# Performance work log

Hardware: AMD Instinct MI355X
Metric: run time of the kernel (lower is better)

The kernel has to match this reference:

```python
import jax, jax.numpy as jnp
import numpy as np

B, N, C, O, K, D = 32, 2048, 64, 64, 3, 16

def setup_inputs() -> dict:
    key = jax.random.key(0)
    ks = jax.random.split(key, 6)
    x = jax.random.normal(ks[0], (B, N, C), dtype=jnp.float32)
    node_embeddings = jax.random.normal(ks[1], (N, D), dtype=jnp.float32)
    adj_m = jax.random.uniform(ks[2], (N, N), dtype=jnp.float32)
    weights_pool = jax.random.normal(ks[3], (D, K, C, O), dtype=jnp.float32) * 0.1
    bias_pool = jax.random.normal(ks[4], (D, O), dtype=jnp.float32) * 0.1
    sa_weight = jax.random.normal(ks[5], (N, 2 * N), dtype=jnp.float32) * (1.0 / np.sqrt(2 * N))
    return {"x": x, "node_embeddings": node_embeddings, "adj_m": adj_m,
            "weights_pool": weights_pool, "bias_pool": bias_pool, "sa_weight": sa_weight}

def reference(x, node_embeddings, adj_m, weights_pool, bias_pool, sa_weight):
    n = node_embeddings.shape[0]
    # learned adaptive adjacency [N,N]
    supports = jax.nn.softmax(jax.nn.relu(node_embeddings @ node_embeddings.T), axis=1)
    # SpatialAttention: 1x1 conv over 2N channels == matmul with [N,2N] weight
    z = jnp.concatenate([supports, adj_m], axis=1) @ sa_weight.T  # [N,N]
    s2 = jax.nn.sigmoid(z)
    supports = s2 * adj_m + (1.0 - s2) * supports
    # Chebyshev polynomial basis
    support_set = [jnp.eye(n, dtype=supports.dtype), supports]
    for _ in range(2, K):
        support_set.append(2.0 * supports @ support_set[-1] - support_set[-2])
    supports_k = jnp.stack(support_set, axis=0)  # [K,N,N]
    # per-node generated weights/bias from embeddings
    weights = jnp.einsum('nd,dkio->nkio', node_embeddings, weights_pool)  # [N,K,C,O]
    bias = node_embeddings @ bias_pool  # [N,O]
    # graph conv: aggregate then per-node matmul
    x_g = jnp.einsum('knm,bmc->bnkc', supports_k, x)  # [B,N,K,C]
    x_gconv = jnp.einsum('bnki,nkio->bno', x_g, weights) + bias  # [B,N,O]
    return x_gconv
```

## Files before the change

kernel.cpp:

```cpp
#include <hip/hip_runtime.h>


typedef unsigned short u16;
typedef float f32x4 __attribute__((ext_vector_type(4)));
typedef __bf16 bf16x8 __attribute__((ext_vector_type(8)));
typedef unsigned short u16x8 __attribute__((ext_vector_type(8)));

#define PSTRIDE ((size_t)2048 * 2048)

__device__ __forceinline__ u16 f2bf(float f) {
    unsigned u = __float_as_uint(f);
    u += 0x7FFFu + ((u >> 16) & 1u);
    return (u16)(u >> 16);
}
__device__ __forceinline__ float bf2f(u16 h) {
    return __uint_as_float((unsigned)h << 16);
}
__device__ __forceinline__ void gl_lds16(const void* g, void* l) {
    __builtin_amdgcn_global_load_lds(
        (const __attribute__((address_space(1))) unsigned*)g,
        (__attribute__((address_space(3))) unsigned*)l, 16, 0, 0);
}

__global__ __launch_bounds__(256)
void preA(const float* __restrict__ E, const float* __restrict__ adj,
          const float* __restrict__ saw, const float* __restrict__ x,
          const float* __restrict__ Wp, const float* __restrict__ bp,
          u16* __restrict__ Acat, u16* __restrict__ sawb, u16* __restrict__ xtT,
          u16* __restrict__ Wpb, float* __restrict__ Wpbf,
          float* __restrict__ bias, u16* __restrict__ xn, int mode) {
    __shared__ __align__(16) char smem[32768];
    const int bid = blockIdx.x, tid = threadIdx.x;

    if (bid < 256) {
        float* Et4 = (float*)smem;
        const int r0 = bid * 8;
        float z[8][8] = {};
#pragma unroll
        for (int ph = 0; ph < 4; ++ph) {
            if (ph) __syncthreads();
#pragma unroll
            for (int k = 0; k < 8; ++k) {
                const int n = tid + 256 * k;
                float4 e = ((const float4*)(E + (size_t)n * 16))[ph];
                Et4[0 * 2048 + n] = e.x; Et4[1 * 2048 + n] = e.y;
                Et4[2 * 2048 + n] = e.z; Et4[3 * 2048 + n] = e.w;
            }
            __syncthreads();
#pragma unroll
            for (int d = 0; d < 4; ++d) {
                const float* row = Et4 + d * 2048;
                float ev[8];
#pragma unroll
                for (int k = 0; k < 8; ++k) ev[k] = row[tid + 256 * k];
#pragma unroll
                for (int r = 0; r < 8; ++r) {
                    float e = row[r0 + r];
#pragma unroll
                    for (int k = 0; k < 8; ++k) z[r][k] = fmaf(e, ev[k], z[r][k]);
                }
            }
        }
        __syncthreads();
        float (*redm)[8] = (float(*)[8])smem;
        float (*reds)[8] = (float(*)[8])(smem + 256);

        float mr[8];
#pragma unroll
        for (int r = 0; r < 8; ++r) {
            float m = 0.f;
#pragma unroll
            for (int k = 0; k < 8; ++k) { z[r][k] = fmaxf(z[r][k], 0.f); m = fmaxf(m, z[r][k]); }
            mr[r] = m;
        }
#pragma unroll
        for (int off = 32; off; off >>= 1)
#pragma unroll
            for (int r = 0; r < 8; ++r) mr[r] = fmaxf(mr[r], __shfl_xor(mr[r], off, 64));
        if ((tid & 63) == 0) {
#pragma unroll
            for (int r = 0; r < 8; ++r) redm[tid >> 6][r] = mr[r];
        }
        __syncthreads();
#pragma unroll
        for (int r = 0; r < 8; ++r)
            mr[r] = fmaxf(fmaxf(redm[0][r], redm[1][r]), fmaxf(redm[2][r], redm[3][r]));
        float sr[8];
#pragma unroll
        for (int r = 0; r < 8; ++r) {
            float s = 0.f;
#pragma unroll
            for (int k = 0; k < 8; ++k) { z[r][k] = __expf(z[r][k] - mr[r]); s += z[r][k]; }
            sr[r] = s;
        }
#pragma unroll
        for (int off = 32; off; off >>= 1)
#pragma unroll
            for (int r = 0; r < 8; ++r) sr[r] += __shfl_xor(sr[r], off, 64);
        if ((tid & 63) == 0) {
#pragma unroll
            for (int r = 0; r < 8; ++r) reds[tid >> 6][r] = sr[r];
        }
        __syncthreads();
#pragma unroll
        for (int r = 0; r < 8; ++r) {
            float inv = 1.f / (reds[0][r] + reds[1][r] + reds[2][r] + reds[3][r]);
            u16* orow = Acat + (size_t)(r0 + r) * 4096;
#pragma unroll
            for (int k = 0; k < 8; ++k) orow[tid + 256 * k] = f2bf(z[r][k] * inv);
        }
    } else if (bid < 1792) {
        const size_t NADJ = 1048576, STRIDE = (size_t)1536 * 256;
        const size_t e0 = (size_t)(bid - 256) * 256 + tid;
        float4 v[8];
#pragma unroll
        for (int it = 0; it < 8; ++it) {
            size_t idx = e0 + (size_t)it * STRIDE;
            const float* src = (idx < NADJ) ? (adj + idx * 4) : (saw + (idx - NADJ) * 4);
            v[it] = *(const float4*)src;
        }
#pragma unroll
        for (int it = 0; it < 8; ++it) {
            size_t idx = e0 + (size_t)it * STRIDE;
            ushort4 o = make_ushort4(f2bf(v[it].x), f2bf(v[it].y), f2bf(v[it].z), f2bf(v[it].w));
            if (idx < NADJ) {
                size_t j = idx * 4;
                int n = (int)(j >> 11), c = (int)(j & 2047);
                *(ushort4*)(Acat + (size_t)n * 4096 + 2048 + c) = o;
            } else {
                *(ushort4*)(sawb + (idx - NADJ) * 4) = o;
            }
        }
    } else if (bid < 2816) {
        u16 (*t)[65] = (u16(*)[65])smem;
        int local = bid - 1792;
        int m0 = (local & 31) * 64, b = local >> 5;
        int c = tid & 63, g = tid >> 6;
#pragma unroll
        for (int r = 0; r < 16; ++r) {
            int mm = g * 16 + r;
            t[mm][c] = f2bf(x[((size_t)b * 2048 + m0 + mm) * 64 + c]);
        }
        __syncthreads();
#pragma unroll
        for (int r = 0; r < 16; ++r) {
            int cc = g * 16 + r;
            xtT[((size_t)b * 64 + cc) * 2048 + m0 + c] = t[c][cc];
        }
        if (mode) {
#pragma unroll
            for (int r = 0; r < 16; ++r) {
                int mm = g * 16 + r;
                xn[((size_t)(m0 + mm)) * 2048 + b * 64 + c] = t[mm][c];
            }
        }
    } else if (bid < 2832) {
        float (*tw)[97] = (float(*)[97])smem;
        const int d = bid - 2816;
        const float* base = Wp + (size_t)d * 12288;
        const int o = tid & 63, seg = tid >> 6;
#pragma unroll
        for (int half = 0; half < 2; ++half) {
            if (half) __syncthreads();
#pragma unroll
            for (int j = 0; j < 24; ++j) {
                int ki = half * 96 + seg * 24 + j;
                int k = ki >> 6, i = ki & 63;
                float v;
                if (k == 0)      v = base[i * 64 + o] - base[8192 + i * 64 + o];
                else if (k == 1) v = base[4096 + i * 64 + o];
                else             v = 2.f * base[8192 + i * 64 + o];
                tw[o][ki - half * 96] = v;
            }
            __syncthreads();
#pragma unroll
            for (int it = 0; it < 6; ++it) {
                int idx = tid + it * 256;
                int oo = idx / 24, q = idx - oo * 24;
                float v0 = tw[oo][q * 4], v1 = tw[oo][q * 4 + 1];
                float v2 = tw[oo][q * 4 + 2], v3 = tw[oo][q * 4 + 3];
                size_t dst = (size_t)(d * 64 + oo) * 192 + half * 96 + q * 4;
                *(float4*)(Wpbf + dst) = make_float4(v0, v1, v2, v3);
                *(ushort4*)(Wpb + dst) = make_ushort4(f2bf(v0), f2bf(v1), f2bf(v2), f2bf(v3));
            }
        }
    } else {
        const int nb = bid - 2832;
#pragma unroll
        for (int it = 0; it < 8; ++it) {
            int idx = tid + it * 256;
            int n = nb * 32 + (idx >> 6), o = idx & 63;
            float s = 0.f;
#pragma unroll
            for (int d = 0; d < 16; ++d) s = fmaf(E[n * 16 + d], bp[d * 64 + o], s);
            bias[(size_t)n * 64 + o] = s;
        }
    }
}

__global__ __launch_bounds__(256)
void rzmid(const u16* __restrict__ p, const u16* __restrict__ Acat,
           u16* __restrict__ S, const float* __restrict__ E,
           const float* __restrict__ Wpbf, u16* __restrict__ Wnb) {
    __shared__ float Es[32 * 16];
    const int bid = blockIdx.x, tid = threadIdx.x;
    if (bid < 1024) {
        const size_t base = ((size_t)bid * 256 + tid) * 4;
        const size_t STRIDE = (size_t)1024 * 256 * 4;
#pragma unroll
        for (int it = 0; it < 4; ++it) {
            size_t j = base + (size_t)it * STRIDE;
            ushort4 p0 = *(const ushort4*)(p + j);
            ushort4 p1 = *(const ushort4*)(p + PSTRIDE + j);
            ushort4 p2 = *(const ushort4*)(p + 2 * PSTRIDE + j);
            ushort4 p3 = *(const ushort4*)(p + 3 * PSTRIDE + j);
            int row = (int)(j >> 11), col = (int)(j & 2047);
            ushort4 sp = *(const ushort4*)(Acat + (size_t)row * 4096 + col);
            ushort4 ad = *(const ushort4*)(Acat + (size_t)row * 4096 + 2048 + col);
            float z0 = bf2f(p0.x) + bf2f(p1.x) + bf2f(p2.x) + bf2f(p3.x);
            float z1 = bf2f(p0.y) + bf2f(p1.y) + bf2f(p2.y) + bf2f(p3.y);
            float z2 = bf2f(p0.z) + bf2f(p1.z) + bf2f(p2.z) + bf2f(p3.z);
            float z3 = bf2f(p0.w) + bf2f(p1.w) + bf2f(p2.w) + bf2f(p3.w);
            float s0 = 1.f / (1.f + __expf(-z0)), s1 = 1.f / (1.f + __expf(-z1));
            float s2 = 1.f / (1.f + __expf(-z2)), s3 = 1.f / (1.f + __expf(-z3));
            ushort4 o = make_ushort4(
                f2bf(s0 * bf2f(ad.x) + (1.f - s0) * bf2f(sp.x)),
                f2bf(s1 * bf2f(ad.y) + (1.f - s1) * bf2f(sp.y)),
                f2bf(s2 * bf2f(ad.z) + (1.f - s2) * bf2f(sp.z)),
                f2bf(s3 * bf2f(ad.w) + (1.f - s3) * bf2f(sp.w)));
            *(ushort4*)(S + j) = o;
        }
    } else {
        const int w = bid - 1024;
        const int c0 = (w % 12) * 1024, n0 = (w / 12) * 32;
        for (int j = tid; j < 512; j += 256) Es[j] = E[(size_t)n0 * 16 + j];
        float4 wf[16];
#pragma unroll
        for (int d = 0; d < 16; ++d)
            wf[d] = *(const float4*)(Wpbf + (size_t)d * 12288 + c0 + tid * 4);
        __syncthreads();
        for (int nl = 0; nl < 32; ++nl) {
            float4 s = make_float4(0.f, 0.f, 0.f, 0.f);
#pragma unroll
            for (int d = 0; d < 16; ++d) {
                float e = Es[nl * 16 + d];
                s.x = fmaf(e, wf[d].x, s.x);
                s.y = fmaf(e, wf[d].y, s.y);
                s.z = fmaf(e, wf[d].z, s.z);
                s.w = fmaf(e, wf[d].w, s.w);
            }
            *(ushort4*)(Wnb + (size_t)(n0 + nl) * 12288 + c0 + tid * 4) =
                make_ushort4(f2bf(s.x), f2bf(s.y), f2bf(s.z), f2bf(s.w));
        }
    }
}

__global__ __launch_bounds__(512, 2)
void gemm_bt256(const u16* __restrict__ A, const u16* __restrict__ Bt,
                u16* __restrict__ Cp, int M, int N, int K, int Kh) {
    __shared__ alignas(16) u16 As[2][256 * 64];
    __shared__ alignas(16) u16 Bs[2][256 * 64];
    const int tid = threadIdx.x, lane = tid & 63, wave = tid >> 6;

    const int nbx = gridDim.x, nby = gridDim.y, nbz = gridDim.z;
    const int nwg = nbx * nby * nbz;
    int lin = (blockIdx.z * nby + blockIdx.y) * nbx + blockIdx.x;
    if ((nwg & 7) == 0) lin = (lin & 7) * (nwg >> 3) + (lin >> 3);
    const int bz = lin / (nbx * nby);
    const int r2 = lin - bz * nbx * nby;
    const int by = r2 / nbx, bx = r2 - by * nbx;

    const int m0 = by * 256, n0 = bx * 256;
    const int kbeg = bz * Kh;
    const int NT = Kh >> 6;
    const int wm = (wave >> 2) * 128, wn = (wave & 3) * 64;
    const int ml = lane & 15, c0l = lane >> 4;

    int sI[4], rowI[4], gcI[4];
#pragma unroll
    for (int r = 0; r < 4; ++r) {
        int s = r * 512 + tid;
        sI[r] = s; rowI[r] = s >> 3; gcI[r] = (s & 7) ^ ((s >> 3) & 7);
    }

    f32x4 acc[8][4] = {};
    bf16x8 af[4][2], bv[2][2];

#define LOADA(r_, kt_, buf_) \
    gl_lds16(A + (size_t)(m0 + rowI[r_]) * K + (kt_) + gcI[r_] * 8, \
             &As[buf_][sI[r_] * 8])
#define LOADB(r_, kt_, buf_) \
    gl_lds16(Bt + (size_t)(n0 + rowI[r_]) * K + (kt_) + gcI[r_] * 8, \
             &Bs[buf_][sI[r_] * 8])

#define DSRA(qa_) \
    _Pragma("unroll") \
    for (int i = 0; i < 4; ++i) { \
        const int mr = wm + (qa_) * 64 + i * 16 + ml; \
        _Pragma("unroll") \
        for (int ks = 0; ks < 2; ++ks) \
            af[i][ks] = *(const bf16x8*)(Asc + mr * 64 + (((c0l + ks * 4) ^ (mr & 7)) * 8)); \
    }
#define DSRB(qb_) \
    _Pragma("unroll") \
    for (int j = 0; j < 2; ++j) { \
        const int nr = wn + (qb_) * 32 + j * 16 + ml; \
        _Pragma("unroll") \
        for (int ks = 0; ks < 2; ++ks) \
            bv[j][ks] = *(const bf16x8*)(Bsc + nr * 64 + (((c0l + ks * 4) ^ (nr & 7)) * 8)); \
    }
#define MMQ(io_, jo_) \
    __builtin_amdgcn_s_barrier(); \
    asm volatile("s_waitcnt lgkmcnt(0)" ::: "memory"); \
    __builtin_amdgcn_s_setprio(1); \
    _Pragma("unroll") \
    for (int ks = 0; ks < 2; ++ks) \
        _Pragma("unroll") \
        for (int i = 0; i < 4; ++i) \
            _Pragma("unroll") \
            for (int j = 0; j < 2; ++j) \
                acc[(io_) + i][(jo_) + j] = __builtin_amdgcn_mfma_f32_16x16x32_bf16( \
                    af[i][ks], bv[j][ks], acc[(io_) + i][(jo_) + j], 0, 0, 0); \
    __builtin_amdgcn_s_setprio(0);

#pragma unroll
    for (int r = 0; r < 4; ++r) LOADA(r, kbeg, 0);
#pragma unroll
    for (int r = 0; r < 4; ++r) LOADB(r, kbeg, 0);
    asm volatile("s_waitcnt vmcnt(0)" ::: "memory");
    __builtin_amdgcn_s_barrier();

    for (int t = 0; t < NT - 1; ++t) {
        const int cur = t & 1, nxt = cur ^ 1;
        const u16* Asc = As[cur];
        const u16* Bsc = Bs[cur];
        const int k1 = kbeg + (t + 1) * 64;

        DSRA(0); DSRB(0);
        LOADB(0, k1, nxt); LOADB(1, k1, nxt);
        MMQ(0, 0);
        __builtin_amdgcn_s_barrier();

        DSRB(1);
        LOADB(2, k1, nxt); LOADB(3, k1, nxt);
        MMQ(0, 2);
        asm volatile("s_waitcnt vmcnt(4)" ::: "memory");
        __builtin_amdgcn_s_barrier();

        DSRA(1);
        LOADA(0, k1, nxt); LOADA(2, k1, nxt);
        MMQ(4, 2);
        __builtin_amdgcn_s_barrier();

        DSRB(0);
        LOADA(1, k1, nxt); LOADA(3, k1, nxt);
        MMQ(4, 0);
        asm volatile("s_waitcnt vmcnt(2)" ::: "memory");
        __builtin_amdgcn_s_barrier();
    }

    {
        const int cur = (NT - 1) & 1;
        const u16* Asc = As[cur];
        const u16* Bsc = Bs[cur];

        DSRA(0); DSRB(0);
        MMQ(0, 0);
        __builtin_amdgcn_s_barrier();

        DSRB(1);
        MMQ(0, 2);
        asm volatile("s_waitcnt vmcnt(0)" ::: "memory");
        __builtin_amdgcn_s_barrier();

        DSRA(1);
        MMQ(4, 2);
        __builtin_amdgcn_s_barrier();

        DSRB(0);
        MMQ(4, 0);
    }

#undef LOADA
#undef LOADB
#undef DSRA
#undef DSRB
#undef MMQ

    const int col_l = lane & 15, rl = (lane >> 4) * 4;
    u16* Cz = Cp + (size_t)bz * M * N;
#pragma unroll
    for (int i = 0; i < 8; ++i)
#pragma unroll
        for (int j = 0; j < 4; ++j)
#pragma unroll
            for (int r = 0; r < 4; ++r) {
                int row = m0 + wm + i * 16 + rl + r;
                int col = n0 + wn + j * 16 + col_l;
                Cz[(size_t)row * N + col] = f2bf(acc[i][j][r]);
            }
}

__global__ __launch_bounds__(256)
void reduceT(const u16* __restrict__ p, u16* __restrict__ xg1o,
             u16* __restrict__ xg1T, int mode) {
    __shared__ u16 t[64][68];
    int bx = blockIdx.x * 64, by = blockIdx.y * 64;
    int cg = threadIdx.x & 15, rg = threadIdx.x >> 4;
    int b = bx >> 6;
#pragma unroll
    for (int rr = 0; rr < 4; ++rr) {
        int row = rg * 4 + rr;
        size_t idx = (size_t)(by + row) * 2048 + bx + cg * 4;
        ushort4 q0 = *(const ushort4*)(p + idx);
        ushort4 q1 = *(const ushort4*)(p + PSTRIDE + idx);
        ushort4 q2 = *(const ushort4*)(p + 2 * PSTRIDE + idx);
        ushort4 q3 = *(const ushort4*)(p + 3 * PSTRIDE + idx);
        ushort4 v = make_ushort4(
            f2bf(bf2f(q0.x) + bf2f(q1.x) + bf2f(q2.x) + bf2f(q3.x)),
            f2bf(bf2f(q0.y) + bf2f(q1.y) + bf2f(q2.y) + bf2f(q3.y)),
            f2bf(bf2f(q0.z) + bf2f(q1.z) + bf2f(q2.z) + bf2f(q3.z)),
            f2bf(bf2f(q0.w) + bf2f(q1.w) + bf2f(q2.w) + bf2f(q3.w)));
        if (mode) *(ushort4*)(xg1o + idx) = v;
        else      *(ushort4*)(xg1o + ((size_t)b * 2048 + by + row) * 64 + cg * 4) = v;
        *(ushort4*)(&t[row][cg * 4]) = v;
    }
    __syncthreads();
    int c = threadIdx.x & 63, g = threadIdx.x >> 6;
#pragma unroll
    for (int r = 0; r < 16; ++r) {
        int row = g * 16 + r;
        xg1T[(size_t)(bx + row) * 2048 + by + c] = t[c][row];
    }
}

__global__ __launch_bounds__(256, 4)
void gconv_wn(const u16* __restrict__ xn, const u16* __restrict__ xg1n,
              const u16* __restrict__ p, const u16* __restrict__ Wnb,
              const float* __restrict__ bias, float* __restrict__ out) {
    __shared__ alignas(16) u16 As[32 * 192];
    __shared__ alignas(16) u16 Bs[64 * 192];
    const int n = blockIdx.x, tid = threadIdx.x;
    const int lane = tid & 63, wave = tid >> 6;
    const int wn2 = wave * 16;
    const int ml = lane & 15, c0l = lane >> 4;
    const int col = lane & 15, rl = (lane >> 4) * 4;

#pragma unroll
    for (int it = 0; it < 6; ++it) {
        int s = tid + it * 256;
        int row = s / 24, sc = s - row * 24;
        int gc = (sc & 24) | ((sc ^ row) & 7);
        gl_lds16(Wnb + (size_t)n * 12288 + (size_t)row * 192 + gc * 8, Bs + (size_t)s * 8);
    }
#pragma unroll
    for (int it = 0; it < 3; ++it) {
        int s = tid + it * 256;
        int row = s / 24, sc = s - row * 24;
        int gc = (sc & 24) | ((sc ^ row) & 7);
        u16x8 v;
        if (gc < 8) {
            v = *(const u16x8*)(xn + (size_t)n * 2048 + row * 64 + (gc & 7) * 8);
        } else if (gc < 16) {
            v = *(const u16x8*)(xg1n + (size_t)n * 2048 + row * 64 + (gc & 7) * 8);
        } else {
            const u16* pp = p + (size_t)n * 2048 + row * 64 + (gc & 7) * 8;
            u16x8 q0 = *(const u16x8*)pp;
            u16x8 q1 = *(const u16x8*)(pp + PSTRIDE);
            u16x8 q2 = *(const u16x8*)(pp + 2 * PSTRIDE);
            u16x8 q3 = *(const u16x8*)(pp + 3 * PSTRIDE);
#pragma unroll
            for (int tt = 0; tt < 8; ++tt)
                v[tt] = f2bf(bf2f(q0[tt]) + bf2f(q1[tt]) + bf2f(q2[tt]) + bf2f(q3[tt]));
        }
        *(u16x8*)(As + (size_t)s * 8) = v;
    }
    float bv0 = bias[(size_t)n * 64 + wn2 + col];
    f32x4 acc[2];
#pragma unroll
    for (int mt = 0; mt < 2; ++mt)
#pragma unroll
        for (int r = 0; r < 4; ++r) acc[mt][r] = bv0;
    __syncthreads();

#pragma unroll
    for (int ks = 0; ks < 6; ++ks) {
        int c = c0l + ks * 4;
        int o = wn2 + ml;
        bf16x8 bfrag = *(const bf16x8*)(Bs + (o * 24 + ((c & 24) | ((c ^ (o & 7)) & 7))) * 8);
#pragma unroll
        for (int mt = 0; mt < 2; ++mt) {
            int m = mt * 16 + ml;
            bf16x8 afrag = *(const bf16x8*)(As + (m * 24 + ((c & 24) | ((c ^ (m & 7)) & 7))) * 8);
            acc[mt] = __builtin_amdgcn_mfma_f32_16x16x32_bf16(afrag, bfrag, acc[mt], 0, 0, 0);
        }
    }
#pragma unroll
    for (int mt = 0; mt < 2; ++mt)
#pragma unroll
        for (int r = 0; r < 4; ++r) {
            int b = mt * 16 + rl + r;
            out[((size_t)b * 2048 + n) * 64 + wn2 + col] = acc[mt][r];
        }
}

__global__ __launch_bounds__(256, 2)
void gconv_mfma(const float* __restrict__ x, const u16* __restrict__ xg1,
                const u16* __restrict__ p, const u16* __restrict__ Wpb,
                const float* __restrict__ bias, const float* __restrict__ E,
                float* __restrict__ out) {
    __shared__ alignas(16) float El[16 * 128];
    const int tid = threadIdx.x, lane = tid & 63, wave = tid >> 6;
    const int m0 = blockIdx.x * 128, nb = m0 & 2047, bB = m0 >> 11;
    const int wm = (wave >> 1) * 64, wn = (wave & 1) * 32;
    const int ml = lane & 15, c0l = lane >> 4;
    const int col_l = lane & 15, rl = (lane >> 4) * 4;

#pragma unroll
    for (int it = 0; it < 8; ++it) {
        int idx = tid + it * 256;
        El[idx] = E[(size_t)(nb + (idx & 127)) * 16 + (idx >> 7)];
    }
    __syncthreads();

    bf16x8 af[4][6];
#pragma unroll
    for (int i = 0; i < 4; ++i) {
        const int row = m0 + wm + i * 16 + ml;
        const int n = row & 2047;
#pragma unroll
        for (int ks = 0; ks < 2; ++ks) {
            const float* xp = x + (size_t)row * 64 + (c0l + ks * 4) * 8;
            float4 a = *(const float4*)xp, b4 = *(const float4*)(xp + 4);
            u16x8 v;
            v[0] = f2bf(a.x);  v[1] = f2bf(a.y);  v[2] = f2bf(a.z);  v[3] = f2bf(a.w);
            v[4] = f2bf(b4.x); v[5] = f2bf(b4.y); v[6] = f2bf(b4.z); v[7] = f2bf(b4.w);
            af[i][ks] = __builtin_bit_cast(bf16x8, v);
        }
#pragma unroll
        for (int ks = 2; ks < 4; ++ks)
            af[i][ks] = *(const bf16x8*)(xg1 + (size_t)row * 64 + (c0l + ks * 4 - 8) * 8);
#pragma unroll
        for (int ks = 4; ks < 6; ++ks) {
            const u16* pp = p + (size_t)n * 2048 + bB * 64 + (c0l + ks * 4 - 16) * 8;
            u16x8 q0 = *(const u16x8*)pp;
            u16x8 q1 = *(const u16x8*)(pp + PSTRIDE);
            u16x8 q2 = *(const u16x8*)(pp + 2 * PSTRIDE);
            u16x8 q3 = *(const u16x8*)(pp + 3 * PSTRIDE);
            u16x8 v;
#pragma unroll
            for (int tt = 0; tt < 8; ++tt)
                v[tt] = f2bf(bf2f(q0[tt]) + bf2f(q1[tt]) + bf2f(q2[tt]) + bf2f(q3[tt]));
            af[i][ks] = __builtin_bit_cast(bf16x8, v);
        }
    }

    f32x4 oacc[4][2];
#pragma unroll
    for (int i = 0; i < 4; ++i)
#pragma unroll
        for (int j = 0; j < 2; ++j)
#pragma unroll
            for (int r = 0; r < 4; ++r)
                oacc[i][j][r] = bias[(size_t)(nb + wm + i * 16 + rl + r) * 64 + wn + j * 16 + col_l];

#pragma unroll 2
    for (int d = 0; d < 16; ++d) {
        bf16x8 bv[2][6];
#pragma unroll
        for (int j = 0; j < 2; ++j) {
            const u16* wp = Wpb + (size_t)(d * 64 + wn + j * 16 + ml) * 192 + c0l * 8;
#pragma unroll
            for (int ks = 0; ks < 6; ++ks)
                bv[j][ks] = *(const bf16x8*)(wp + ks * 32);
        }
        f32x4 tmp[4][2] = {};
#pragma unroll
        for (int ks = 0; ks < 6; ++ks)
#pragma unroll
            for (int i = 0; i < 4; ++i)
#pragma unroll
                for (int j = 0; j < 2; ++j)
                    tmp[i][j] = __builtin_amdgcn_mfma_f32_16x16x32_bf16(af[i][ks], bv[j][ks], tmp[i][j], 0, 0, 0);
#pragma unroll
        for (int i = 0; i < 4; ++i) {
            f32x4 ev = *(const f32x4*)(El + d * 128 + wm + i * 16 + rl);
#pragma unroll
            for (int r = 0; r < 4; ++r)
#pragma unroll
                for (int j = 0; j < 2; ++j)
                    oacc[i][j][r] = fmaf(ev[r], tmp[i][j][r], oacc[i][j][r]);
        }
    }
#pragma unroll
    for (int i = 0; i < 4; ++i)
#pragma unroll
        for (int j = 0; j < 2; ++j)
#pragma unroll
            for (int r = 0; r < 4; ++r)
                out[(size_t)(m0 + wm + i * 16 + rl + r) * 64 + wn + j * 16 + col_l] = oacc[i][j][r];
}

extern "C" void kernel_launch(void* const* d_in, const int* in_sizes, int n_in,
                              void* d_out, int out_size, void* d_ws, size_t ws_size,
                              hipStream_t stream) {
    const float* x   = (const float*)d_in[0];
    const float* E   = (const float*)d_in[1];
    const float* adj = (const float*)d_in[2];
    const float* Wp  = (const float*)d_in[3];
    const float* bp  = (const float*)d_in[4];
    const float* saw = (const float*)d_in[5];
    float* out = (float*)d_out;

    char* ws = (char*)d_ws;
    const size_t MB = 1u << 20;
    const int wn_mode = (ws_size >= 140 * MB) ? 1 : 0;

    u16*   Acat  = (u16*)(ws);
    u16*   sawb  = (u16*)(ws + 16 * MB);
    u16*   XtT   = (u16*)(ws + 32 * MB);
    u16*   Wpb   = (u16*)(ws + 40 * MB);
    float* bias  = (float*)(ws + 41 * MB);
    float* Wpbf  = (float*)(ws + 42 * MB);
    u16*   part  = (u16*)(ws + 48 * MB);
    u16*   S_bf  = (u16*)(ws + 16 * MB);
    u16*   xg1T  = (u16*)(ws + 24 * MB);
    u16*   xg1o  = (u16*)(ws);
    u16*   xn    = (u16*)(ws + 80 * MB);
    u16*   Wnb   = (u16*)(ws + 88 * MB);

    preA<<<2896, 256, 0, stream>>>(E, adj, saw, x, Wp, bp, Acat, sawb, XtT,
                                   Wpb, Wpbf, bias, xn, wn_mode);

    gemm_bt256<<<dim3(8, 8, 4), 512, 0, stream>>>(Acat, sawb, part, 2048, 2048, 4096, 1024);
    rzmid<<<wn_mode ? 1792 : 1024, 256, 0, stream>>>(part, Acat, S_bf, E, Wpbf, Wnb);
    gemm_bt256<<<dim3(8, 8, 4), 512, 0, stream>>>(S_bf, XtT, part, 2048, 2048, 2048, 512);
    reduceT<<<dim3(32, 32), 256, 0, stream>>>(part, xg1o, xg1T, wn_mode);
    gemm_bt256<<<dim3(8, 8, 4), 512, 0, stream>>>(S_bf, xg1T, part, 2048, 2048, 2048, 512);

    if (wn_mode)
        gconv_wn<<<2048, 256, 0, stream>>>(xn, xg1o, part, Wnb, bias, out);
    else
        gconv_mfma<<<512, 256, 0, stream>>>(x, xg1o, part, Wpb, bias, E, out);
}
```

Baseline: 274.7 us.

## Split preprocessing kernel into memory-bound and compute-bound kernels, move Wnb generation earlier

Moves the embedding softmax work and the per-node weight generation (Wnb) out of the mixed preprocessing and reduction kernels into a new kernel, zsmW, launched before the first GEMM. The remaining conversion work goes into preB, which uses less LDS and a 4-blocks-per-CU launch bound so more blocks can be resident, and it processes more elements per block in the adj/saw conversion. The sigmoid-blend reduction becomes a lean standalone kernel. This adds one kernel launch in exchange for better occupancy and less branch divergence across heterogeneous blocks.

```diff
diff --git a/kernel.cpp b/kernel.cpp
--- a/kernel.cpp
+++ b/kernel.cpp
@@ -22,105 +22,70 @@
         (__attribute__((address_space(3))) unsigned*)l, 16, 0, 0);
 }
 
-__global__ __launch_bounds__(256)
-void preA(const float* __restrict__ E, const float* __restrict__ adj,
+__global__ __launch_bounds__(256, 4)
+void preB(const float* __restrict__ E, const float* __restrict__ adj,
           const float* __restrict__ saw, const float* __restrict__ x,
           const float* __restrict__ Wp, const float* __restrict__ bp,
           u16* __restrict__ Acat, u16* __restrict__ sawb, u16* __restrict__ xtT,
           u16* __restrict__ Wpb, float* __restrict__ Wpbf,
           float* __restrict__ bias, u16* __restrict__ xn, int mode) {
-    __shared__ __align__(16) char smem[32768];
+    __shared__ __align__(16) char smem[12800];
     const int bid = blockIdx.x, tid = threadIdx.x;
 
-    if (bid < 256) {
-        float* Et4 = (float*)smem;
-        const int r0 = bid * 8;
-        float z[8][8] = {};
-#pragma unroll
-        for (int ph = 0; ph < 4; ++ph) {
-            if (ph) __syncthreads();
-#pragma unroll
-            for (int k = 0; k < 8; ++k) {
-                const int n = tid + 256 * k;
-                float4 e = ((const float4*)(E + (size_t)n * 16))[ph];
-                Et4[0 * 2048 + n] = e.x; Et4[1 * 2048 + n] = e.y;
-                Et4[2 * 2048 + n] = e.z; Et4[3 * 2048 + n] = e.w;
+    if (bid < 16) {
+        float (*tw)[49] = (float(*)[49])smem;
+        const int d = bid;
+        const float* base = Wp + (size_t)d * 12288;
+        const int o = tid & 63, seg = tid >> 6;
+#pragma unroll
+        for (int p = 0; p < 4; ++p) {
+            if (p) __syncthreads();
+#pragma unroll
+            for (int j = 0; j < 12; ++j) {
+                int kil = seg * 12 + j;
+                int ki = p * 48 + kil;
+                int k = ki >> 6, i = ki & 63;
+                float v;
+                if (k == 0)      v = base[i * 64 + o] - base[8192 + i * 64 + o];
+                else if (k == 1) v = base[4096 + i * 64 + o];
+                else             v = 2.f * base[8192 + i * 64 + o];
+                tw[o][kil] = v;
             }
             __syncthreads();
 #pragma unroll
-            for (int d = 0; d < 4; ++d) {
-                const float* row = Et4 + d * 2048;
-                float ev[8];
-#pragma unroll
-                for (int k = 0; k < 8; ++k) ev[k] = row[tid + 256 * k];
-#pragma unroll
-                for (int r = 0; r < 8; ++r) {
-                    float e = row[r0 + r];
-#pragma unroll
-                    for (int k = 0; k < 8; ++k) z[r][k] = fmaf(e, ev[k], z[r][k]);
-                }
-            }
-        }
-        __syncthreads();
-        float (*redm)[8] = (float(*)[8])smem;
-        float (*reds)[8] = (float(*)[8])(smem + 256);
-
-        float mr[8];
-#pragma unroll
-        for (int r = 0; r < 8; ++r) {
-            float m = 0.f;
-#pragma unroll
-            for (int k = 0; k < 8; ++k) { z[r][k] = fmaxf(z[r][k], 0.f); m = fmaxf(m, z[r][k]); }
-            mr[r] = m;
-        }
-#pragma unroll
-        for (int off = 32; off; off >>= 1)
-#pragma unroll
-            for (int r = 0; r < 8; ++r) mr[r] = fmaxf(mr[r], __shfl_xor(mr[r], off, 64));
-        if ((tid & 63) == 0) {
-#pragma unroll
-            for (int r = 0; r < 8; ++r) redm[tid >> 6][r] = mr[r];
-        }
-        __syncthreads();
-#pragma unroll
-        for (int r = 0; r < 8; ++r)
-            mr[r] = fmaxf(fmaxf(redm[0][r], redm[1][r]), fmaxf(redm[2][r], redm[3][r]));
-        float sr[8];
-#pragma unroll
-        for (int r = 0; r < 8; ++r) {
+            for (int it = 0; it < 3; ++it) {
+                int idx = tid + it * 256;
+                int oo = idx / 12, q = idx - oo * 12;
+                float v0 = tw[oo][q * 4], v1 = tw[oo][q * 4 + 1];
+                float v2 = tw[oo][q * 4 + 2], v3 = tw[oo][q * 4 + 3];
+                size_t dst = (size_t)(d * 64 + oo) * 192 + p * 48 + q * 4;
+                *(float4*)(Wpbf + dst) = make_float4(v0, v1, v2, v3);
+                *(ushort4*)(Wpb + dst) = make_ushort4(f2bf(v0), f2bf(v1), f2bf(v2), f2bf(v3));
+            }
+        }
+    } else if (bid < 80) {
+        const int nb = bid - 16;
+#pragma unroll
+        for (int it = 0; it < 8; ++it) {
+            int idx = tid + it * 256;
+            int n = nb * 32 + (idx >> 6), o = idx & 63;
             float s = 0.f;
 #pragma unroll
-            for (int k = 0; k < 8; ++k) { z[r][k] = __expf(z[r][k] - mr[r]); s += z[r][k]; }
-            sr[r] = s;
-        }
-#pragma unroll
-        for (int off = 32; off; off >>= 1)
-#pragma unroll
-            for (int r = 0; r < 8; ++r) sr[r] += __shfl_xor(sr[r], off, 64);
-        if ((tid & 63) == 0) {
-#pragma unroll
-            for (int r = 0; r < 8; ++r) reds[tid >> 6][r] = sr[r];
-        }
-        __syncthreads();
-#pragma unroll
-        for (int r = 0; r < 8; ++r) {
-            float inv = 1.f / (reds[0][r] + reds[1][r] + reds[2][r] + reds[3][r]);
-            u16* orow = Acat + (size_t)(r0 + r) * 4096;
-#pragma unroll
-            for (int k = 0; k < 8; ++k) orow[tid + 256 * k] = f2bf(z[r][k] * inv);
-        }
-    } else if (bid < 1792) {
-        const size_t NADJ = 1048576, STRIDE = (size_t)1536 * 256;
-        const size_t e0 = (size_t)(bid - 256) * 256 + tid;
-        float4 v[8];
-#pragma unroll
-        for (int it = 0; it < 8; ++it) {
+            for (int d = 0; d < 16; ++d) s = fmaf(E[n * 16 + d], bp[d * 64 + o], s);
+            bias[(size_t)n * 64 + o] = s;
+        }
+    } else if (bid < 848) {
+        const size_t NADJ = 1048576, STRIDE = (size_t)768 * 256;
+        const size_t e0 = (size_t)(bid - 80) * 256 + tid;
+        float4 v[16];
+#pragma unroll
+        for (int it = 0; it < 16; ++it) {
             size_t idx = e0 + (size_t)it * STRIDE;
             const float* src = (idx < NADJ) ? (adj + idx * 4) : (saw + (idx - NADJ) * 4);
             v[it] = *(const float4*)src;
         }
 #pragma unroll
-        for (int it = 0; it < 8; ++it) {
+        for (int it = 0; it < 16; ++it) {
             size_t idx = e0 + (size_t)it * STRIDE;
             ushort4 o = make_ushort4(f2bf(v[it].x), f2bf(v[it].y), f2bf(v[it].z), f2bf(v[it].w));
             if (idx < NADJ) {
@@ -131,9 +96,9 @@
                 *(ushort4*)(sawb + (idx - NADJ) * 4) = o;
             }
         }
-    } else if (bid < 2816) {
+    } else {
         u16 (*t)[65] = (u16(*)[65])smem;
-        int local = bid - 1792;
+        int local = bid - 848;
         int m0 = (local & 31) * 64, b = local >> 5;
         int c = tid & 63, g = tid >> 6;
 #pragma unroll
@@ -154,84 +119,95 @@
                 xn[((size_t)(m0 + mm)) * 2048 + b * 64 + c] = t[mm][c];
             }
         }
-    } else if (bid < 2832) {
-        float (*tw)[97] = (float(*)[97])smem;
-        const int d = bid - 2816;
-        const float* base = Wp + (size_t)d * 12288;
-        const int o = tid & 63, seg = tid >> 6;
-#pragma unroll
-        for (int half = 0; half < 2; ++half) {
-            if (half) __syncthreads();
-#pragma unroll
-            for (int j = 0; j < 24; ++j) {
-                int ki = half * 96 + seg * 24 + j;
-                int k = ki >> 6, i = ki & 63;
-                float v;
-                if (k == 0)      v = base[i * 64 + o] - base[8192 + i * 64 + o];
-                else if (k == 1) v = base[4096 + i * 64 + o];
-                else             v = 2.f * base[8192 + i * 64 + o];
-                tw[o][ki - half * 96] = v;
+    }
+}
+
+__global__ __launch_bounds__(256)
+void zsmW(const float* __restrict__ E, const float* __restrict__ Wpbf,
+          u16* __restrict__ Acat, u16* __restrict__ Wnb) {
+    __shared__ __align__(16) char smem[32768];
+    const int bid = blockIdx.x, tid = threadIdx.x;
+
+    if (bid < 256) {
+        float* Et4 = (float*)smem;
+        const int r0 = bid * 8;
+        float z[8][8] = {};
+#pragma unroll
+        for (int ph = 0; ph < 4; ++ph) {
+            if (ph) __syncthreads();
+#pragma unroll
+            for (int k = 0; k < 8; ++k) {
+                const int n = tid + 256 * k;
+                float4 e = ((const float4*)(E + (size_t)n * 16))[ph];
+                Et4[0 * 2048 + n] = e.x; Et4[1 * 2048 + n] = e.y;
+                Et4[2 * 2048 + n] = e.z; Et4[3 * 2048 + n] = e.w;
             }
             __syncthreads();
 #pragma unroll
-            for (int it = 0; it < 6; ++it) {
-                int idx = tid + it * 256;
-                int oo = idx / 24, q = idx - oo * 24;
-                float v0 = tw[oo][q * 4], v1 = tw[oo][q * 4 + 1];
-                float v2 = tw[oo][q * 4 + 2], v3 = tw[oo][q * 4 + 3];
-                size_t dst = (size_t)(d * 64 + oo) * 192 + half * 96 + q * 4;
-                *(float4*)(Wpbf + dst) = make_float4(v0, v1, v2, v3);
-                *(ushort4*)(Wpb + dst) = make_ushort4(f2bf(v0), f2bf(v1), f2bf(v2), f2bf(v3));
-            }
+            for (int d = 0; d < 4; ++d) {
+                const float* row = Et4 + d * 2048;
+                float ev[8];
+#pragma unroll
+                for (int k = 0; k < 8; ++k) ev[k] = row[tid + 256 * k];
+#pragma unroll
+                for (int r = 0; r < 8; ++r) {
+                    float e = row[r0 + r];
+#pragma unroll
+                    for (int k = 0; k < 8; ++k) z[r][k] = fmaf(e, ev[k], z[r][k]);
+                }
+            }
+        }
+        __syncthreads();
+        float (*redm)[8] = (float(*)[8])smem;
+        float (*reds)[8] = (float(*)[8])(smem + 256);
+
+        float mr[8];
+#pragma unroll
+        for (int r = 0; r < 8; ++r) {
+            float m = 0.f;
+#pragma unroll
+            for (int k = 0; k < 8; ++k) { z[r][k] = fmaxf(z[r][k], 0.f); m = fmaxf(m, z[r][k]); }
+            mr[r] = m;
+        }
+#pragma unroll
+        for (int off = 32; off; off >>= 1)
+#pragma unroll
+            for (int r = 0; r < 8; ++r) mr[r] = fmaxf(mr[r], __shfl_xor(mr[r], off, 64));
+        if ((tid & 63) == 0) {
+#pragma unroll
+            for (int r = 0; r < 8; ++r) redm[tid >> 6][r] = mr[r];
+        }
+        __syncthreads();
+#pragma unroll
+        for (int r = 0; r < 8; ++r)
+            mr[r] = fmaxf(fmaxf(redm[0][r], redm[1][r]), fmaxf(redm[2][r], redm[3][r]));
+        float sr[8];
+#pragma unroll
+        for (int r = 0; r < 8; ++r) {
+            float s = 0.f;
+#pragma unroll
+            for (int k = 0; k < 8; ++k) { z[r][k] = __expf(z[r][k] - mr[r]); s += z[r][k]; }
+            sr[r] = s;
+        }
+#pragma unroll
+        for (int off = 32; off; off >>= 1)
+#pragma unroll
+            for (int r = 0; r < 8; ++r) sr[r] += __shfl_xor(sr[r], off, 64);
+        if ((tid & 63) == 0) {
+#pragma unroll
+            for (int r = 0; r < 8; ++r) reds[tid >> 6][r] = sr[r];
+        }
+        __syncthreads();
+#pragma unroll
+        for (int r = 0; r < 8; ++r) {
+            float inv = 1.f / (reds[0][r] + reds[1][r] + reds[2][r] + reds[3][r]);
+            u16* orow = Acat + (size_t)(r0 + r) * 4096;
+#pragma unroll
+            for (int k = 0; k < 8; ++k) orow[tid + 256 * k] = f2bf(z[r][k] * inv);
         }
     } else {
-        const int nb = bid - 2832;
-#pragma unroll
-        for (int it = 0; it < 8; ++it) {
-            int idx = tid + it * 256;
-            int n = nb * 32 + (idx >> 6), o = idx & 63;
-            float s = 0.f;
-#pragma unroll
-            for (int d = 0; d < 16; ++d) s = fmaf(E[n * 16 + d], bp[d * 64 + o], s);
-            bias[(size_t)n * 64 + o] = s;
-        }
-    }
-}
-
-__global__ __launch_bounds__(256)
-void rzmid(const u16* __restrict__ p, const u16* __restrict__ Acat,
-           u16* __restrict__ S, const float* __restrict__ E,
-           const float* __restrict__ Wpbf, u16* __restrict__ Wnb) {
-    __shared__ float Es[32 * 16];
-    const int bid = blockIdx.x, tid = threadIdx.x;
-    if (bid < 1024) {
-        const size_t base = ((size_t)bid * 256 + tid) * 4;
-        const size_t STRIDE = (size_t)1024 * 256 * 4;
-#pragma unroll
-        for (int it = 0; it < 4; ++it) {
-            size_t j = base + (size_t)it * STRIDE;
-            ushort4 p0 = *(const ushort4*)(p + j);
-            ushort4 p1 = *(const ushort4*)(p + PSTRIDE + j);
-            ushort4 p2 = *(const ushort4*)(p + 2 * PSTRIDE + j);
-            ushort4 p3 = *(const ushort4*)(p + 3 * PSTRIDE + j);
-            int row = (int)(j >> 11), col = (int)(j & 2047);
-            ushort4 sp = *(const ushort4*)(Acat + (size_t)row * 4096 + col);
-            ushort4 ad = *(const ushort4*)(Acat + (size_t)row * 4096 + 2048 + col);
-            float z0 = bf2f(p0.x) + bf2f(p1.x) + bf2f(p2.x) + bf2f(p3.x);
-            float z1 = bf2f(p0.y) + bf2f(p1.y) + bf2f(p2.y) + bf2f(p3.y);
-            float z2 = bf2f(p0.z) + bf2f(p1.z) + bf2f(p2.z) + bf2f(p3.z);
-            float z3 = bf2f(p0.w) + bf2f(p1.w) + bf2f(p2.w) + bf2f(p3.w);
-            float s0 = 1.f / (1.f + __expf(-z0)), s1 = 1.f / (1.f + __expf(-z1));
-            float s2 = 1.f / (1.f + __expf(-z2)), s3 = 1.f / (1.f + __expf(-z3));
-            ushort4 o = make_ushort4(
-                f2bf(s0 * bf2f(ad.x) + (1.f - s0) * bf2f(sp.x)),
-                f2bf(s1 * bf2f(ad.y) + (1.f - s1) * bf2f(sp.y)),
-                f2bf(s2 * bf2f(ad.z) + (1.f - s2) * bf2f(sp.z)),
-                f2bf(s3 * bf2f(ad.w) + (1.f - s3) * bf2f(sp.w)));
-            *(ushort4*)(S + j) = o;
-        }
-    } else {
-        const int w = bid - 1024;
+        float* Es = (float*)smem;
+        const int w = bid - 256;
         const int c0 = (w % 12) * 1024, n0 = (w / 12) * 32;
         for (int j = tid; j < 512; j += 256) Es[j] = E[(size_t)n0 * 16 + j];
         float4 wf[16];
@@ -252,6 +228,36 @@
             *(ushort4*)(Wnb + (size_t)(n0 + nl) * 12288 + c0 + tid * 4) =
                 make_ushort4(f2bf(s.x), f2bf(s.y), f2bf(s.z), f2bf(s.w));
         }
+    }
+}
+
+__global__ __launch_bounds__(256)
+void reduce_z(const u16* __restrict__ p, const u16* __restrict__ Acat,
+              u16* __restrict__ S) {
+    const size_t base = ((size_t)blockIdx.x * 256 + threadIdx.x) * 4;
+    const size_t STRIDE = (size_t)1024 * 256 * 4;
+#pragma unroll
+    for (int it = 0; it < 4; ++it) {
+        size_t j = base + (size_t)it * STRIDE;
+        ushort4 p0 = *(const ushort4*)(p + j);
+        ushort4 p1 = *(const ushort4*)(p + PSTRIDE + j);
+        ushort4 p2 = *(const ushort4*)(p + 2 * PSTRIDE + j);
+        ushort4 p3 = *(const ushort4*)(p + 3 * PSTRIDE + j);
+        int row = (int)(j >> 11), col = (int)(j & 2047);
+        ushort4 sp = *(const ushort4*)(Acat + (size_t)row * 4096 + col);
+        ushort4 ad = *(const ushort4*)(Acat + (size_t)row * 4096 + 2048 + col);
+        float z0 = bf2f(p0.x) + bf2f(p1.x) + bf2f(p2.x) + bf2f(p3.x);
+        float z1 = bf2f(p0.y) + bf2f(p1.y) + bf2f(p2.y) + bf2f(p3.y);
+        float z2 = bf2f(p0.z) + bf2f(p1.z) + bf2f(p2.z) + bf2f(p3.z);
+        float z3 = bf2f(p0.w) + bf2f(p1.w) + bf2f(p2.w) + bf2f(p3.w);
+        float s0 = 1.f / (1.f + __expf(-z0)), s1 = 1.f / (1.f + __expf(-z1));
+        float s2 = 1.f / (1.f + __expf(-z2)), s3 = 1.f / (1.f + __expf(-z3));
+        ushort4 o = make_ushort4(
+            f2bf(s0 * bf2f(ad.x) + (1.f - s0) * bf2f(sp.x)),
+            f2bf(s1 * bf2f(ad.y) + (1.f - s1) * bf2f(sp.y)),
+            f2bf(s2 * bf2f(ad.z) + (1.f - s2) * bf2f(sp.z)),
+            f2bf(s3 * bf2f(ad.w) + (1.f - s3) * bf2f(sp.w)));
+        *(ushort4*)(S + j) = o;
     }
 }
 
@@ -629,11 +635,12 @@
     u16*   xn    = (u16*)(ws + 80 * MB);
     u16*   Wnb   = (u16*)(ws + 88 * MB);
 
-    preA<<<2896, 256, 0, stream>>>(E, adj, saw, x, Wp, bp, Acat, sawb, XtT,
+    preB<<<1872, 256, 0, stream>>>(E, adj, saw, x, Wp, bp, Acat, sawb, XtT,
                                    Wpb, Wpbf, bias, xn, wn_mode);
+    zsmW<<<wn_mode ? 1024 : 256, 256, 0, stream>>>(E, Wpbf, Acat, Wnb);
 
     gemm_bt256<<<dim3(8, 8, 4), 512, 0, stream>>>(Acat, sawb, part, 2048, 2048, 4096, 1024);
-    rzmid<<<wn_mode ? 1792 : 1024, 256, 0, stream>>>(part, Acat, S_bf, E, Wpbf, Wnb);
+    reduce_z<<<1024, 256, 0, stream>>>(part, Acat, S_bf);
     gemm_bt256<<<dim3(8, 8, 4), 512, 0, stream>>>(S_bf, XtT, part, 2048, 2048, 2048, 512);
     reduceT<<<dim3(32, 32), 256, 0, stream>>>(part, xg1o, xg1T, wn_mode);
     gemm_bt256<<<dim3(8, 8, 4), 512, 0, stream>>>(S_bf, xg1T, part, 2048, 2048, 2048, 512);
```

Result: no change. 271.2 us (-1.3%).
